# Kernel optimization log

Hardware: AMD Instinct MI355X
Metric: run time of the kernel (lower is better)

## Reference

```python
import jax, jax.numpy as jnp
import numpy as np

# Dims mirror cfg: hidden_dim=128, n_cluster=512; margin from cfg['memory_bank']
B, D, H, W = 64, 128, 64, 64
K = 512
MARGIN = 0.005
EPS = 1e-12  # F.normalize eps


def setup_inputs() -> dict:
    key = jax.random.key(0)
    k1, k2 = jax.random.split(key)
    x = jax.random.normal(k1, (B, D, H, W), dtype=jnp.float32)
    centroid = jax.random.normal(k2, (K, D), dtype=jnp.float32)
    return {"x": x, "centroid": centroid}


def _l2_normalize(v, axis=-1):
    n = jnp.sqrt(jnp.sum(v * v, axis=axis, keepdims=True))
    return v / jnp.maximum(n, EPS)


def reference(x, centroid):
    b, d, h, w = x.shape
    # _flatten: (b,d,h,w) -> (bhw, d)
    flat_raw = jnp.transpose(x, (0, 2, 3, 1)).reshape(-1, d)  # (N, d)
    norm_x = _l2_normalize(flat_raw)                          # (N, d), F.normalize(dim=-1)
    c_norm = _l2_normalize(centroid)                          # (K, d)

    dist = (jnp.sum(norm_x * norm_x, axis=1, keepdims=True)
            + jnp.sum(c_norm * c_norm, axis=1)
            - 2.0 * jnp.matmul(norm_x, c_norm.T))

    idx = jnp.argmin(dist, axis=-1)                           # (N,) hard assignment
    neg_top2, _ = jax.lax.top_k(-dist, 2)                     # torch.topk(-distance, k=2)
    gap = neg_top2[:, 0] - neg_top2[:, 1]                     # values[:,0]-values[:,1]
    above = gap > MARGIN                                      # margin mask

    # masked per-cluster scatter of the RAW features (the enqueue step),
    # expressed as a fixed-shape segment reduction instead of ragged queues.
    sel = jnp.where(above[:, None], flat_raw, 0.0)            # (N, d)
    cluster_sums = jax.ops.segment_sum(sel, idx, num_segments=K)            # (K, d)
    counts = jax.ops.segment_sum(above.astype(jnp.float32), idx, num_segments=K)  # (K,)

    # _reshape(norm_z1_1): (bhw, d) -> (b, d, h, w)
    out = jnp.transpose(norm_x.reshape(b, h, w, d), (0, 3, 1, 2))
    return out, cluster_sums, counts, idx
```

## Files before the change

kernel.cpp:

```cpp
#include <hip/hip_runtime.h>
#include <stdint.h>

#define D 128
#define K 512
#define HW 4096
#define NPIX 262144
#define OUT_NORM_ELEMS 33554432
#define MARGIN 0.005f
#define EPS 1e-12f
#define LOSCALE 2048.0f
#define RSCALE (1.0f / 2048.0f)

typedef _Float16 f16x8 __attribute__((ext_vector_type(8)));
typedef float f32x4 __attribute__((ext_vector_type(4)));
typedef float f32x2 __attribute__((ext_vector_type(2)));

#define FENCE() asm volatile("" ::: "memory")

__device__ __forceinline__ short f2h(float f) {
    _Float16 h = (_Float16)f; return *reinterpret_cast<short*>(&h);
}
__device__ __forceinline__ float h2f(short s) {
    _Float16 h = *reinterpret_cast<_Float16*>(&s); return (float)h;
}

__global__ void zero_kernel(float* __restrict__ p, int n) {
    int i = blockIdx.x * blockDim.x + threadIdx.x;
    if (i < n) p[i] = 0.0f;
}

__global__ void normalize_centroids(const float* __restrict__ c,
                                    short* __restrict__ csp,
                                    float* __restrict__ nc) {
    int k = blockIdx.x * 4 + (threadIdx.x >> 6);
    int lane = threadIdx.x & 63;
    float2 v = *(const float2*)(c + (size_t)k * D + lane * 2);
    float ss = v.x * v.x + v.y * v.y;
    #pragma unroll
    for (int off = 32; off; off >>= 1) ss += __shfl_xor(ss, off);
    float rinv = 1.0f / fmaxf(sqrtf(ss), EPS);
    float ox = v.x * rinv, oy = v.y * rinv;
    short hx = f2h(ox), hy = f2h(oy);
    short lx = f2h((ox - h2f(hx)) * LOSCALE);
    short ly = f2h((oy - h2f(hy)) * LOSCALE);
    *(short2*)&csp[(size_t)k * 256 + 2 * lane]       = make_short2(hx, hy);
    *(short2*)&csp[(size_t)k * 256 + 128 + 2 * lane] = make_short2(lx, ly);
    float ss2 = ox * ox + oy * oy;
    #pragma unroll
    for (int off = 32; off; off >>= 1) ss2 += __shfl_xor(ss2, off);
    if (lane == 0) nc[k] = ss2;
}

#define K1S 66
__global__ __launch_bounds__(256) void normalize_x(
    const float* __restrict__ x, float* __restrict__ out_norm,
    float* __restrict__ rows, int prim)
{
    __shared__ float xt[256 * K1S];
    const int t = threadIdx.x;
    const int pix0 = blockIdx.x * 256;
    const int b = pix0 >> 12;
    const int p0 = pix0 & (HW - 1);
    const float* xg = x + (size_t)b * (D * HW) + p0 + t;
    float* og = out_norm + (size_t)b * (D * HW) + p0 + t;

    float ss = 0.f;
    #pragma unroll 16
    for (int d = 0; d < D; ++d) { float v = xg[(size_t)d * HW]; ss += v * v; }
    float rinv = 1.f / fmaxf(sqrtf(ss), EPS);

    if (prim) {
        #pragma unroll
        for (int half = 0; half < 2; ++half) {
            const int d0 = half * 64;
            #pragma unroll 8
            for (int d = 0; d < 64; ++d) {
                float v = xg[(size_t)(d0 + d) * HW];
                og[(size_t)(d0 + d) * HW] = v * rinv;
                xt[t * K1S + d] = v;
            }
            __syncthreads();
            #pragma unroll
            for (int s = 0; s < 32; ++s) {
                int idx = s * 256 + t;
                int p = idx >> 5;
                int i = idx & 31;
                f32x2 v = *(f32x2*)&xt[p * K1S + 2 * i];
                *(f32x2*)&rows[(size_t)(pix0 + p) * 128 + d0 + 2 * i] = v;
            }
            __syncthreads();
        }
    } else {
        #pragma unroll 16
        for (int d = 0; d < D; ++d) {
            float v = xg[(size_t)d * HW];
            og[(size_t)d * HW] = v * rinv;
        }
    }
}

#define UPD(dd, cc, ri) do {                                      \
    bool lt1 = (dd) < d1[ri];                                     \
    float nd2 = lt1 ? d1[ri] : (((dd) < d2[ri]) ? (dd) : d2[ri]); \
    i1[ri] = lt1 ? (cc) : i1[ri];                                 \
    d1[ri] = lt1 ? (dd) : d1[ri];                                 \
    d2[ri] = nd2;                                                 \
} while (0)

#define SMBUF 16384
#define SMNC  65536
#define SM2_BYTES 67584
__global__ __launch_bounds__(512, 4) void gemm_top2(
    const float* __restrict__ xn, const float* __restrict__ rows,
    const short* __restrict__ csp, const float* __restrict__ nc,
    float* __restrict__ oidx, int* __restrict__ pixinfo, int prim)
{
    __shared__ char smem[SM2_BYTES] __attribute__((aligned(16)));
    float* nc_s = (float*)(smem + SMNC);

    const int t = threadIdx.x;
    const int lane = t & 63;
    const int wid = t >> 6;
    const int lb15 = lane & 15;
    const int kl4 = lane >> 4;
    const int kl = kl4 * 16;
    const int lswzB = (lb15 & 7) << 4;
    const int pix0 = blockIdx.x * 256;

    nc_s[t] = nc[t];

    auto stageB = [&](int bufoff, int cb) {
        const char* src = (const char*)csp + (size_t)cb * 512;
        #pragma unroll
        for (int r = 0; r < 2; ++r) {
            int P = r * 8192 + wid * 1024;
            int Pl = P + lane * 16;
            int row = Pl >> 9;
            int goff = Pl ^ ((row & 7) << 4);
            __builtin_amdgcn_global_load_lds(
                (const __attribute__((address_space(1))) uint32_t*)(src + goff),
                (__attribute__((address_space(3))) uint32_t*)(smem + bufoff + P),
                16, 0, 0);
        }
    };

    f16x8 ahi[2][4], alo[2][4];
    if (prim) {
        #pragma unroll
        for (int mf = 0; mf < 2; ++mf) {
            const float* rp = rows + (size_t)(pix0 + wid * 32 + mf * 16 + lb15) * 128;
            f32x4 v0[4], v1[4];
            float ss = 0.f;
            #pragma unroll
            for (int kq = 0; kq < 4; ++kq) {
                v0[kq] = *(const f32x4*)(rp + kq * 32 + kl4 * 8);
                v1[kq] = *(const f32x4*)(rp + kq * 32 + kl4 * 8 + 4);
                #pragma unroll
                for (int e = 0; e < 4; ++e)
                    ss += v0[kq][e] * v0[kq][e] + v1[kq][e] * v1[kq][e];
            }
            ss += __shfl_xor(ss, 16);
            ss += __shfl_xor(ss, 32);
            float rinv = 1.f / fmaxf(sqrtf(ss), EPS);
            #pragma unroll
            for (int kq = 0; kq < 4; ++kq) {
                f16x8 h, l;
                #pragma unroll
                for (int e = 0; e < 4; ++e) {
                    float a = v0[kq][e] * rinv;
                    _Float16 hv = (_Float16)a;
                    h[e] = hv; l[e] = (_Float16)((a - (float)hv) * LOSCALE);
                    float c = v1[kq][e] * rinv;
                    _Float16 hw = (_Float16)c;
                    h[4 + e] = hw; l[4 + e] = (_Float16)((c - (float)hw) * LOSCALE);
                }
                ahi[mf][kq] = h; alo[mf][kq] = l;
            }
        }
    } else {
        #pragma unroll
        for (int mf = 0; mf < 2; ++mf) {
            int px = pix0 + wid * 32 + mf * 16 + lb15;
            const float* xp = xn + (size_t)(px >> 12) * (D * HW) + (px & (HW - 1));
            #pragma unroll
            for (int kq = 0; kq < 4; ++kq) {
                f16x8 h, l;
                #pragma unroll
                for (int e = 0; e < 8; ++e) {
                    float v = xp[(size_t)(kq * 32 + kl4 * 8 + e) * HW];
                    _Float16 hv = (_Float16)v;
                    h[e] = hv;
                    l[e] = (_Float16)((v - (float)hv) * LOSCALE);
                }
                ahi[mf][kq] = h; alo[mf][kq] = l;
            }
        }
    }
    __syncthreads();

    stageB(0 * SMBUF, 0);
    stageB(1 * SMBUF, 32);

    float d1[8], d2[8]; int i1[8];
    #pragma unroll
    for (int r = 0; r < 8; ++r) { d1[r] = 3.4e38f; d2[r] = 3.4e38f; i1[r] = 0; }

    for (int c = 0; c < 16; ++c) {
        const int cb = c * 32;
        if (c + 2 < 16) stageB(((c + 2) & 3) * SMBUF, cb + 64);
        if (c < 14)      { asm volatile("s_waitcnt vmcnt(4)" ::: "memory"); }
        else if (c == 14){ asm volatile("s_waitcnt vmcnt(2)" ::: "memory"); }
        else             { asm volatile("s_waitcnt vmcnt(0)" ::: "memory"); }
        __builtin_amdgcn_s_barrier();
        FENCE();
        const int bufoff = (c & 3) * SMBUF;

        f32x4 am[2][2], ac[2][2];
        #pragma unroll
        for (int mf = 0; mf < 2; ++mf)
            #pragma unroll
            for (int nf = 0; nf < 2; ++nf) {
                am[mf][nf] = (f32x4){0.f, 0.f, 0.f, 0.f};
                ac[mf][nf] = (f32x4){0.f, 0.f, 0.f, 0.f};
            }

        #pragma unroll
        for (int kq = 0; kq < 4; ++kq) {
            #pragma unroll
            for (int nf = 0; nf < 2; ++nf) {
                const int rowb = (nf * 16 + lb15) * 512;
                f16x8 bh = *(const f16x8*)(smem + bufoff + rowb + ((kq * 64 + kl) ^ lswzB));
                f16x8 bl = *(const f16x8*)(smem + bufoff + rowb + ((256 + kq * 64 + kl) ^ lswzB));
                #pragma unroll
                for (int mf = 0; mf < 2; ++mf) {
                    am[mf][nf] = __builtin_amdgcn_mfma_f32_16x16x32_f16(ahi[mf][kq], bh, am[mf][nf], 0, 0, 0);
                    ac[mf][nf] = __builtin_amdgcn_mfma_f32_16x16x32_f16(ahi[mf][kq], bl, ac[mf][nf], 0, 0, 0);
                    ac[mf][nf] = __builtin_amdgcn_mfma_f32_16x16x32_f16(alo[mf][kq], bh, ac[mf][nf], 0, 0, 0);
                }
            }
        }

        #pragma unroll
        for (int nf = 0; nf < 2; ++nf) {
            int cid = cb + nf * 16 + lb15;
            float ncv = nc_s[cid];
            #pragma unroll
            for (int mf = 0; mf < 2; ++mf)
                #pragma unroll
                for (int j = 0; j < 4; ++j) {
                    int ri = mf * 4 + j;
                    float dd = ncv - 2.f * am[mf][nf][j] - (2.f * RSCALE) * ac[mf][nf][j];
                    UPD(dd, cid, ri);
                }
        }
        FENCE();
    }

    #pragma unroll
    for (int r = 0; r < 8; ++r) {
        #pragma unroll
        for (int m = 1; m < 16; m <<= 1) {
            float o1 = __shfl_xor(d1[r], m);
            float o2 = __shfl_xor(d2[r], m);
            int   oi = __shfl_xor(i1[r], m);
            bool take = (o1 < d1[r]) || (o1 == d1[r] && oi < i1[r]);
            float loser = take ? d1[r] : o1;
            d2[r] = fminf(loser, fminf(d2[r], o2));
            if (take) { d1[r] = o1; i1[r] = oi; }
        }
    }
    if (lb15 == 0) {
        #pragma unroll
        for (int mf = 0; mf < 2; ++mf)
            #pragma unroll
            for (int j = 0; j < 4; ++j) {
                int r = mf * 4 + j;
                int px = pix0 + wid * 32 + mf * 16 + kl4 * 4 + j;
                oidx[px] = (float)i1[r];
                pixinfo[px] = (d2[r] - d1[r] > MARGIN) ? i1[r] : -1;
            }
    }
}

__global__ __launch_bounds__(256) void segsum_kernel(
    const float* __restrict__ x, const float* __restrict__ rows,
    const int* __restrict__ pixinfo, float* __restrict__ csum,
    float* __restrict__ ccnt, int prim)
{
    __shared__ float psum[4 * 128];
    __shared__ int pcnt[4];
    const int kc   = blockIdx.x >> 2;
    const int qtr  = blockIdx.x & 3;
    const int lane = threadIdx.x & 63;
    const int w    = threadIdx.x >> 6;
    const int base = qtr * 65536 + w * 16384;

    float a0 = 0.f, a1 = 0.f;
    int cnt = 0;
    for (int it = 0; it < 256; ++it) {
        int ibase = base + it * 64;
        int v = pixinfo[ibase + lane];
        unsigned long long m = __ballot(v == kc);
        cnt += (int)__popcll(m);
        while (m) {
            int bpos = __builtin_ctzll(m);
            m &= m - 1;
            int pid = ibase + bpos;
            if (prim) {
                f32x2 r = *(const f32x2*)(rows + (size_t)pid * 128 + 2 * lane);
                a0 += r.x;
                a1 += r.y;
            } else {
                const float* xp = x + ((size_t)(pid >> 12)) * (D * HW) + (pid & (HW - 1));
                a0 += xp[(size_t)(2 * lane) * HW];
                a1 += xp[(size_t)(2 * lane + 1) * HW];
            }
        }
    }
    psum[w * 128 + 2 * lane]     = a0;
    psum[w * 128 + 2 * lane + 1] = a1;
    if (lane == 0) pcnt[w] = cnt;
    __syncthreads();
    if (threadIdx.x < 128) {
        float s = psum[threadIdx.x] + psum[128 + threadIdx.x] +
                  psum[256 + threadIdx.x] + psum[384 + threadIdx.x];
        atomicAdd(&csum[(size_t)kc * D + threadIdx.x], s);
    }
    if (threadIdx.x == 0) {
        float c = (float)(pcnt[0] + pcnt[1] + pcnt[2] + pcnt[3]);
        atomicAdd(&ccnt[kc], c);
    }
}

extern "C" void kernel_launch(void* const* d_in, const int* in_sizes, int n_in,
                              void* d_out, int out_size, void* d_ws, size_t ws_size,
                              hipStream_t stream) {
    const float* x   = (const float*)d_in[0];
    const float* cen = (const float*)d_in[1];

    float* out      = (float*)d_out;
    float* out_norm = out;
    float* csum     = out + OUT_NORM_ELEMS;
    float* ccnt     = csum + (size_t)K * D;
    float* oidx     = ccnt + K;

    char* ws = (char*)d_ws;
    short* csp     = (short*)ws;
    float* nc      = (float*)(ws + 262144);
    int*   pixinfo = (int*)(ws + 264192);
    float* rows    = (float*)(ws + 1312768);
    const size_t need_prim = 1312768ull + (size_t)NPIX * D * 4;
    int prim = (ws_size >= need_prim) ? 1 : 0;

    hipLaunchKernelGGL(zero_kernel, dim3((K * D + K + 255) / 256), dim3(256), 0, stream,
                       csum, K * D + K);
    hipLaunchKernelGGL(normalize_centroids, dim3(K / 4), dim3(256), 0, stream,
                       cen, csp, nc);
    hipLaunchKernelGGL(normalize_x, dim3(NPIX / 256), dim3(256), 0, stream,
                       x, out_norm, rows, prim);
    hipLaunchKernelGGL(gemm_top2, dim3(NPIX / 256), dim3(512), 0, stream,
                       out_norm, rows, csp, nc, oidx, pixinfo, prim);
    hipLaunchKernelGGL(segsum_kernel, dim3(K * 4), dim3(256), 0, stream,
                       x, rows, pixinfo, csum, ccnt, prim);
}
```

Before: 351.2 us.

## Double-buffer centroid tiles in pairs, prefetch early, and raise MFMA priority

Restructures the centroid-tile pipeline in gemm_top2. Instead of four rotating 16KB buffers with a wait and barrier per 32-centroid chunk, it uses two 32KB pair buffers with one wait and barrier per 64 centroids. The first two tiles are now issued before the pixel-row (A) loads so that their fetch overlaps A staging. The MFMA block is wrapped in s_setprio to favour matrix issue. This halves the number of barriers, but each prefetch now only has one pair of compute to hide behind before a full vmcnt(0) drain.

```diff
diff --git a/kernel.cpp b/kernel.cpp
--- a/kernel.cpp
+++ b/kernel.cpp
@@ -107,8 +107,8 @@
     d2[ri] = nd2;                                                 \
 } while (0)
 
-#define SMBUF 16384
-#define SMNC  65536
+#define SMPAIR 32768
+#define SMNC   65536
 #define SM2_BYTES 67584
 __global__ __launch_bounds__(512, 4) void gemm_top2(
     const float* __restrict__ xn, const float* __restrict__ rows,
@@ -144,6 +144,9 @@
         }
     };
 
+    stageB(0, 0);
+    stageB(16384, 32);
+
     f16x8 ahi[2][4], alo[2][4];
     if (prim) {
         #pragma unroll
@@ -198,62 +201,71 @@
     }
     __syncthreads();
 
-    stageB(0 * SMBUF, 0);
-    stageB(1 * SMBUF, 32);
+    stageB(32768, 64);
+    stageB(49152, 96);
 
     float d1[8], d2[8]; int i1[8];
     #pragma unroll
     for (int r = 0; r < 8; ++r) { d1[r] = 3.4e38f; d2[r] = 3.4e38f; i1[r] = 0; }
 
-    for (int c = 0; c < 16; ++c) {
-        const int cb = c * 32;
-        if (c + 2 < 16) stageB(((c + 2) & 3) * SMBUF, cb + 64);
-        if (c < 14)      { asm volatile("s_waitcnt vmcnt(4)" ::: "memory"); }
-        else if (c == 14){ asm volatile("s_waitcnt vmcnt(2)" ::: "memory"); }
-        else             { asm volatile("s_waitcnt vmcnt(0)" ::: "memory"); }
-        __builtin_amdgcn_s_barrier();
-        FENCE();
-        const int bufoff = (c & 3) * SMBUF;
-
-        f32x4 am[2][2], ac[2][2];
-        #pragma unroll
-        for (int mf = 0; mf < 2; ++mf)
+    for (int p = 0; p < 8; ++p) {
+        if (p >= 1 && p + 1 < 8) {
+            stageB(((p + 1) & 1) * SMPAIR,         (p + 1) * 64);
+            stageB(((p + 1) & 1) * SMPAIR + 16384, (p + 1) * 64 + 32);
+        }
+
+        #pragma unroll
+        for (int q = 0; q < 2; ++q) {
+            const int cb = p * 64 + q * 32;
+            const int bufoff = (p & 1) * SMPAIR + q * 16384;
+
+            f32x4 am[2][2], ac[2][2];
+            #pragma unroll
+            for (int mf = 0; mf < 2; ++mf)
+                #pragma unroll
+                for (int nf = 0; nf < 2; ++nf) {
+                    am[mf][nf] = (f32x4){0.f, 0.f, 0.f, 0.f};
+                    ac[mf][nf] = (f32x4){0.f, 0.f, 0.f, 0.f};
+                }
+
+            __builtin_amdgcn_s_setprio(1);
+            #pragma unroll
+            for (int kq = 0; kq < 4; ++kq) {
+                #pragma unroll
+                for (int nf = 0; nf < 2; ++nf) {
+                    const int rowb = (nf * 16 + lb15) * 512;
+                    f16x8 bh = *(const f16x8*)(smem + bufoff + rowb + ((kq * 64 + kl) ^ lswzB));
+                    f16x8 bl = *(const f16x8*)(smem + bufoff + rowb + ((256 + kq * 64 + kl) ^ lswzB));
+                    #pragma unroll
+                    for (int mf = 0; mf < 2; ++mf) {
+                        am[mf][nf] = __builtin_amdgcn_mfma_f32_16x16x32_f16(ahi[mf][kq], bh, am[mf][nf], 0, 0, 0);
+                        ac[mf][nf] = __builtin_amdgcn_mfma_f32_16x16x32_f16(ahi[mf][kq], bl, ac[mf][nf], 0, 0, 0);
+                        ac[mf][nf] = __builtin_amdgcn_mfma_f32_16x16x32_f16(alo[mf][kq], bh, ac[mf][nf], 0, 0, 0);
+                    }
+                }
+            }
+            __builtin_amdgcn_s_setprio(0);
+
             #pragma unroll
             for (int nf = 0; nf < 2; ++nf) {
-                am[mf][nf] = (f32x4){0.f, 0.f, 0.f, 0.f};
-                ac[mf][nf] = (f32x4){0.f, 0.f, 0.f, 0.f};
-            }
-
-        #pragma unroll
-        for (int kq = 0; kq < 4; ++kq) {
-            #pragma unroll
-            for (int nf = 0; nf < 2; ++nf) {
-                const int rowb = (nf * 16 + lb15) * 512;
-                f16x8 bh = *(const f16x8*)(smem + bufoff + rowb + ((kq * 64 + kl) ^ lswzB));
-                f16x8 bl = *(const f16x8*)(smem + bufoff + rowb + ((256 + kq * 64 + kl) ^ lswzB));
-                #pragma unroll
-                for (int mf = 0; mf < 2; ++mf) {
-                    am[mf][nf] = __builtin_amdgcn_mfma_f32_16x16x32_f16(ahi[mf][kq], bh, am[mf][nf], 0, 0, 0);
-                    ac[mf][nf] = __builtin_amdgcn_mfma_f32_16x16x32_f16(ahi[mf][kq], bl, ac[mf][nf], 0, 0, 0);
-                    ac[mf][nf] = __builtin_amdgcn_mfma_f32_16x16x32_f16(alo[mf][kq], bh, ac[mf][nf], 0, 0, 0);
-                }
-            }
-        }
-
-        #pragma unroll
-        for (int nf = 0; nf < 2; ++nf) {
-            int cid = cb + nf * 16 + lb15;
-            float ncv = nc_s[cid];
-            #pragma unroll
-            for (int mf = 0; mf < 2; ++mf)
-                #pragma unroll
-                for (int j = 0; j < 4; ++j) {
-                    int ri = mf * 4 + j;
-                    float dd = ncv - 2.f * am[mf][nf][j] - (2.f * RSCALE) * ac[mf][nf][j];
-                    UPD(dd, cid, ri);
-                }
-        }
-        FENCE();
+                int cid = cb + nf * 16 + lb15;
+                float ncv = nc_s[cid];
+                #pragma unroll
+                for (int mf = 0; mf < 2; ++mf)
+                    #pragma unroll
+                    for (int j = 0; j < 4; ++j) {
+                        int ri = mf * 4 + j;
+                        float dd = ncv - 2.f * am[mf][nf][j] - (2.f * RSCALE) * ac[mf][nf][j];
+                        UPD(dd, cid, ri);
+                    }
+            }
+        }
+
+        if (p < 7) {
+            asm volatile("s_waitcnt vmcnt(0)" ::: "memory");
+            __builtin_amdgcn_s_barrier();
+            FENCE();
+        }
     }
 
     #pragma unroll
```

Measured after the change: 633.0 us. +80.2%, slower.

## Prefetch first centroid tiles earlier and interleave MFMA with per-tile argmin update

Applied to the files above, without the earlier changes.

The first two centroid tile loads into LDS are now issued before the A-fragment normalization and load phase instead of after the barrier. This lets those global-to-LDS copies overlap with the pixel loads. The MFMA loop is reordered so each 16-column group is accumulated and then immediately reduced into the running top-2. This halves live accumulators and lets VALU epilogue work overlap the next group's MFMAs. s_setprio is raised around the MFMA block to favour matrix issue across waves. The risk is that the moved stageB now runs before the __syncthreads that previously guarded the LDS buffers.

```diff
diff --git a/kernel.cpp b/kernel.cpp
--- a/kernel.cpp
+++ b/kernel.cpp
@@ -144,6 +144,9 @@
         }
     };
 
+    stageB(0 * SMBUF, 0);
+    stageB(1 * SMBUF, 32);
+
     f16x8 ahi[2][4], alo[2][4];
     if (prim) {
         #pragma unroll
@@ -198,9 +201,6 @@
     }
     __syncthreads();
 
-    stageB(0 * SMBUF, 0);
-    stageB(1 * SMBUF, 32);
-
     float d1[8], d2[8]; int i1[8];
     #pragma unroll
     for (int r = 0; r < 8; ++r) { d1[r] = 3.4e38f; d2[r] = 3.4e38f; i1[r] = 0; }
@@ -215,43 +215,37 @@
         FENCE();
         const int bufoff = (c & 3) * SMBUF;
 
-        f32x4 am[2][2], ac[2][2];
-        #pragma unroll
-        for (int mf = 0; mf < 2; ++mf)
-            #pragma unroll
-            for (int nf = 0; nf < 2; ++nf) {
-                am[mf][nf] = (f32x4){0.f, 0.f, 0.f, 0.f};
-                ac[mf][nf] = (f32x4){0.f, 0.f, 0.f, 0.f};
-            }
-
-        #pragma unroll
-        for (int kq = 0; kq < 4; ++kq) {
-            #pragma unroll
-            for (int nf = 0; nf < 2; ++nf) {
-                const int rowb = (nf * 16 + lb15) * 512;
+        #pragma unroll
+        for (int nf = 0; nf < 2; ++nf) {
+            f32x4 am0 = (f32x4){0.f, 0.f, 0.f, 0.f};
+            f32x4 am1 = (f32x4){0.f, 0.f, 0.f, 0.f};
+            f32x4 ac0 = (f32x4){0.f, 0.f, 0.f, 0.f};
+            f32x4 ac1 = (f32x4){0.f, 0.f, 0.f, 0.f};
+            const int rowb = (nf * 16 + lb15) * 512;
+
+            __builtin_amdgcn_s_setprio(1);
+            #pragma unroll
+            for (int kq = 0; kq < 4; ++kq) {
                 f16x8 bh = *(const f16x8*)(smem + bufoff + rowb + ((kq * 64 + kl) ^ lswzB));
                 f16x8 bl = *(const f16x8*)(smem + bufoff + rowb + ((256 + kq * 64 + kl) ^ lswzB));
-                #pragma unroll
-                for (int mf = 0; mf < 2; ++mf) {
-                    am[mf][nf] = __builtin_amdgcn_mfma_f32_16x16x32_f16(ahi[mf][kq], bh, am[mf][nf], 0, 0, 0);
-                    ac[mf][nf] = __builtin_amdgcn_mfma_f32_16x16x32_f16(ahi[mf][kq], bl, ac[mf][nf], 0, 0, 0);
-                    ac[mf][nf] = __builtin_amdgcn_mfma_f32_16x16x32_f16(alo[mf][kq], bh, ac[mf][nf], 0, 0, 0);
-                }
-            }
-        }
-
-        #pragma unroll
-        for (int nf = 0; nf < 2; ++nf) {
+                am0 = __builtin_amdgcn_mfma_f32_16x16x32_f16(ahi[0][kq], bh, am0, 0, 0, 0);
+                ac0 = __builtin_amdgcn_mfma_f32_16x16x32_f16(ahi[0][kq], bl, ac0, 0, 0, 0);
+                ac0 = __builtin_amdgcn_mfma_f32_16x16x32_f16(alo[0][kq], bh, ac0, 0, 0, 0);
+                am1 = __builtin_amdgcn_mfma_f32_16x16x32_f16(ahi[1][kq], bh, am1, 0, 0, 0);
+                ac1 = __builtin_amdgcn_mfma_f32_16x16x32_f16(ahi[1][kq], bl, ac1, 0, 0, 0);
+                ac1 = __builtin_amdgcn_mfma_f32_16x16x32_f16(alo[1][kq], bh, ac1, 0, 0, 0);
+            }
+            __builtin_amdgcn_s_setprio(0);
+
             int cid = cb + nf * 16 + lb15;
             float ncv = nc_s[cid];
             #pragma unroll
-            for (int mf = 0; mf < 2; ++mf)
-                #pragma unroll
-                for (int j = 0; j < 4; ++j) {
-                    int ri = mf * 4 + j;
-                    float dd = ncv - 2.f * am[mf][nf][j] - (2.f * RSCALE) * ac[mf][nf][j];
-                    UPD(dd, cid, ri);
-                }
+            for (int j = 0; j < 4; ++j) {
+                float dd0 = ncv - 2.f * am0[j] - (2.f * RSCALE) * ac0[j];
+                UPD(dd0, cid, j);
+                float dd1 = ncv - 2.f * am1[j] - (2.f * RSCALE) * ac1[j];
+                UPD(dd1, cid, 4 + j);
+            }
         }
         FENCE();
     }
```

After: 551.3 us. 1.57x slower.
